# Kernel tuning notes

Measured on AMD Instinct MI355X. Metric: run time of the kernel, lower is better.

Reference implementation:

```python
import jax, jax.numpy as jnp
import numpy as np

N_NODES = 100000
N_EDGES = 1600000
EMB = 128
EDGE_DIMS = [6, 3]
BN_EPS = 1e-5


def setup_inputs() -> dict:
    key = jax.random.key(0)
    ks = jax.random.split(key, 16)
    inp = {
        "node_feats": jax.random.normal(ks[0], (N_NODES, EMB), jnp.float32),
        "edge_feat_0": jax.random.uniform(ks[1], (N_EDGES, EDGE_DIMS[0]), jnp.float32),
        "edge_feat_1": jax.random.uniform(ks[2], (N_EDGES, EDGE_DIMS[1]), jnp.float32),
        "src": jax.random.randint(ks[3], (N_EDGES,), 0, N_NODES, jnp.int32),
        "dst": jax.random.randint(ks[4], (N_EDGES,), 0, N_NODES, jnp.int32),
    }
    # edge embedding linears (MLP num_layers==1 -> plain Linear)
    s0 = 1.0 / np.sqrt(EDGE_DIMS[0])
    s1 = 1.0 / np.sqrt(EDGE_DIMS[1])
    inp["We0"] = jax.random.uniform(ks[5], (EDGE_DIMS[0], EMB), jnp.float32, -s0, s0)
    inp["be0"] = jax.random.uniform(ks[6], (EMB,), jnp.float32, -s0, s0)
    inp["We1"] = jax.random.uniform(ks[7], (EDGE_DIMS[1], EMB), jnp.float32, -s1, s1)
    inp["be1"] = jax.random.uniform(ks[8], (EMB,), jnp.float32, -s1, s1)
    # mlp: Linear(emb, 2*emb) -> ReLU -> Linear(2*emb, emb)
    sm = 1.0 / np.sqrt(EMB)
    sh = 1.0 / np.sqrt(2 * EMB)
    inp["W1"] = jax.random.uniform(ks[9], (EMB, 2 * EMB), jnp.float32, -sm, sm)
    inp["b1"] = jax.random.uniform(ks[10], (2 * EMB,), jnp.float32, -sm, sm)
    inp["W2"] = jax.random.uniform(ks[11], (2 * EMB, EMB), jnp.float32, -sh, sh)
    inp["b2"] = jax.random.uniform(ks[12], (EMB,), jnp.float32, -sh, sh)
    # batch norm affine params
    inp["gamma"] = jnp.ones((EMB,), jnp.float32)
    inp["beta"] = jnp.zeros((EMB,), jnp.float32)
    return inp


def reference(node_feats, edge_feat_0, edge_feat_1, src, dst,
              We0, be0, We1, be1, W1, b1, W2, b2, gamma, beta):
    n_nodes = node_feats.shape[0]
    # per-family edge embeddings, summed
    edge_embs = (edge_feat_0 @ We0 + be0) + (edge_feat_1 @ We1 + be1)  # [E, D]
    # u_add_e: gather src node feats, add edge emb
    msgs = node_feats[src] + edge_embs  # [E, D]
    # scatter-sum to destination nodes
    agg = jax.ops.segment_sum(msgs, dst, num_segments=n_nodes)  # [N, D]
    # MLP: Linear -> ReLU -> Linear
    h = jax.nn.relu(agg @ W1 + b1) @ W2 + b2  # [N, D]
    # BatchNorm1d (training mode: batch statistics, biased variance)
    mean = jnp.mean(h, axis=0)
    var = jnp.var(h, axis=0)
    h = (h - mean) * jax.lax.rsqrt(var + BN_EPS) * gamma + beta
    return h
```

## Files before the change

### kernel.cpp

```cpp
#include <hip/hip_runtime.h>

#define N_NODES 100000
#define N_EDGES 1600000
#define EMB 128
#define BM 16
#define NSLAB 64
#define BN_EPS 1e-5f

#define SCAN_BLK 512
#define NB_SCAN ((N_NODES + SCAN_BLK - 1) / SCAN_BLK)
#define NPAD (NB_SCAN * SCAN_BLK)

typedef short short8 __attribute__((ext_vector_type(8)));
typedef float floatx4 __attribute__((ext_vector_type(4)));

__device__ __forceinline__ ushort f2bf(float x) {
    unsigned u = __float_as_uint(x);
    u += 0x7fffu + ((u >> 16) & 1u);
    return (ushort)(u >> 16);
}
__device__ __forceinline__ float lo2f(unsigned p) {
    return __uint_as_float(p << 16);
}
__device__ __forceinline__ float hi2f(unsigned p) {
    return __uint_as_float(p & 0xffff0000u);
}

#define DPP_ADD(x, ctrl, mask) \
    ((x) + __int_as_float(__builtin_amdgcn_update_dpp(0, __float_as_int(x), ctrl, mask, 0xf, true)))

__device__ __forceinline__ float wave_sum63(float x) {
    x = DPP_ADD(x, 0x111, 0xf);
    x = DPP_ADD(x, 0x112, 0xf);
    x = DPP_ADD(x, 0x114, 0xf);
    x = DPP_ADD(x, 0x118, 0xf);
    x = DPP_ADD(x, 0x142, 0xa);
    x = DPP_ADD(x, 0x143, 0xc);
    return __int_as_float(__builtin_amdgcn_readlane(__float_as_int(x), 63));
}

__global__ __launch_bounds__(256) void setup_kernel(
    const float* __restrict__ nf, ushort* __restrict__ nfbf,
    const int* __restrict__ dst, int* __restrict__ counts,
    const float* __restrict__ W1, const float* __restrict__ W2,
    ushort* __restrict__ w1f, ushort* __restrict__ w2f)
{
    int gtid = blockIdx.x * 256 + threadIdx.x;
    long gstride = (long)gridDim.x * 256;

    if (gtid < 65536) {
        int idx = gtid;
        int i = idx & 7;
        int lane = (idx >> 3) & 63;
        int kloc = ((lane >> 4) << 3) + i;
        int nloc = lane & 15;
        if (idx < 32768) {
            int ks = (idx >> 9) & 3, nt = idx >> 11;
            w1f[idx] = f2bf(W1[(ks * 32 + kloc) * 256 + nt * 16 + nloc]);
        } else {
            int j = idx - 32768;
            int ks = (j >> 9) & 7, nt = j >> 12;
            w2f[j] = f2bf(W2[(ks * 32 + kloc) * 128 + nt * 16 + nloc]);
        }
    }

    long total = (long)N_NODES * EMB / 4;
    for (long p = gtid; p < total; p += gstride) {
        float4 v = ((const float4*)nf)[p];
        ushort4 o;
        o.x = f2bf(v.x); o.y = f2bf(v.y); o.z = f2bf(v.z); o.w = f2bf(v.w);
        ((ushort4*)nfbf)[p] = o;
    }

    for (long e = gtid; e < N_EDGES; e += gstride)
        atomicAdd(&counts[dst[e]], 1);
}

__global__ __launch_bounds__(SCAN_BLK) void scan_blocksum_kernel(
    const int* __restrict__ counts, int* __restrict__ blockSums)
{
    __shared__ int red[SCAN_BLK];
    int t = threadIdx.x;
    int i = blockIdx.x * SCAN_BLK + t;
    red[t] = (i < N_NODES) ? counts[i] : 0;
    __syncthreads();
    for (int s = SCAN_BLK / 2; s > 0; s >>= 1) {
        if (t < s) red[t] += red[t + s];
        __syncthreads();
    }
    if (t == 0) blockSums[blockIdx.x] = red[0];
}

__global__ __launch_bounds__(SCAN_BLK) void scan_final_kernel(
    const int* __restrict__ counts, const int* __restrict__ blockSums,
    int* __restrict__ offsets, int* __restrict__ cursor)
{
    __shared__ int s[SCAN_BLK];
    __shared__ int bs[256];
    int t = threadIdx.x;
    if (t < 256) bs[t] = (t < NB_SCAN) ? blockSums[t] : 0;
    __syncthreads();
    for (int off = 1; off < 256; off <<= 1) {
        int v = (t < 256 && t >= off) ? bs[t - off] : 0;
        __syncthreads();
        if (t < 256) bs[t] += v;
        __syncthreads();
    }
    int blockBase = (blockIdx.x == 0) ? 0 : bs[blockIdx.x - 1];

    int i = blockIdx.x * SCAN_BLK + t;
    int orig = (i < N_NODES) ? counts[i] : 0;
    s[t] = orig;
    __syncthreads();
    for (int off = 1; off < SCAN_BLK; off <<= 1) {
        int v = (t >= off) ? s[t - off] : 0;
        __syncthreads();
        s[t] += v;
        __syncthreads();
    }
    int excl = s[t] - orig + blockBase;
    if (i < N_NODES) { offsets[i] = excl; cursor[i] = excl; }
    if (i == N_NODES) offsets[N_NODES] = N_EDGES;
}

__global__ __launch_bounds__(256) void scatter24_kernel(
    const int* __restrict__ src, const int* __restrict__ dst,
    const float* __restrict__ ef0, const float* __restrict__ ef1,
    int* __restrict__ cursor, int* __restrict__ rec24)
{
    int e = blockIdx.x * 256 + threadIdx.x;
    if (e >= N_EDGES) return;
    int t = dst[e];
    int pos = atomicAdd(&cursor[t], 1);

    const float2* p0 = (const float2*)(ef0 + (long)e * 6);
    float2 q0 = p0[0], q1 = p0[1], q2 = p0[2];
    const float* p1 = ef1 + (long)e * 3;
    float g0 = p1[0], g1 = p1[1], g2 = p1[2];

    unsigned u0 = (unsigned)f2bf(q0.x) | ((unsigned)f2bf(q0.y) << 16);
    unsigned u1 = (unsigned)f2bf(q1.x) | ((unsigned)f2bf(q1.y) << 16);
    unsigned u2 = (unsigned)f2bf(q2.x) | ((unsigned)f2bf(q2.y) << 16);
    unsigned u3 = (unsigned)f2bf(g0)   | ((unsigned)f2bf(g1) << 16);
    unsigned u4 = (unsigned)f2bf(g2);

    int2* out = (int2*)(rec24 + (long)pos * 6);
    out[0] = make_int2(src[e], (int)u0);
    out[1] = make_int2((int)u1, (int)u2);
    out[2] = make_int2((int)u3, (int)u4);
}

__device__ __forceinline__ void gather_full_chunks(
    int& base, int end, int lane, int q, int lp,
    const int* __restrict__ rec24, const int4* __restrict__ nf16,
    float4& accA, float4& accB, float* fs)
{
    for (; base + 64 <= end; base += 64) {
        const int2* rp = (const int2*)(rec24 + (long)(base + lane) * 6);
        int2 ra = rp[0], rb = rp[1], rc = rp[2];
        int sid = ra.x;
        fs[0] += lo2f((unsigned)ra.y); fs[1] += hi2f((unsigned)ra.y);
        fs[2] += lo2f((unsigned)rb.x); fs[3] += hi2f((unsigned)rb.x);
        fs[4] += lo2f((unsigned)rb.y); fs[5] += hi2f((unsigned)rb.y);
        fs[6] += lo2f((unsigned)rc.x); fs[7] += hi2f((unsigned)rc.x);
        fs[8] += lo2f((unsigned)rc.y);
#pragma unroll 4
        for (int j = 0; j < 16; ++j) {
            int s = __shfl(sid, 4 * j + q);
            int4 nv = nf16[(long)s * 16 + lp];
            accA.x += lo2f((unsigned)nv.x); accA.y += hi2f((unsigned)nv.x);
            accA.z += lo2f((unsigned)nv.y); accA.w += hi2f((unsigned)nv.y);
            accB.x += lo2f((unsigned)nv.z); accB.y += hi2f((unsigned)nv.z);
            accB.z += lo2f((unsigned)nv.w); accB.w += hi2f((unsigned)nv.w);
        }
    }
}

__global__ __launch_bounds__(256, 8) void gather4_kernel(
    const ushort* __restrict__ nfbf, const int* __restrict__ rec24,
    const int* __restrict__ offsets,
    const float* __restrict__ We0, const float* __restrict__ be0,
    const float* __restrict__ We1, const float* __restrict__ be1,
    float* __restrict__ agg)
{
    int wv = threadIdx.x >> 6, lane = threadIdx.x & 63;
    int n0 = blockIdx.x * 8 + wv * 2;
    int q = lane >> 4, lp = lane & 15;
    const int4* nf16 = (const int4*)nfbf;

    int beg0 = offsets[n0];
    int mid  = offsets[n0 + 1];
    int end1 = offsets[n0 + 2];

    float4 a0A = make_float4(0.f, 0.f, 0.f, 0.f), a0B = a0A;
    float4 a1A = a0A, a1B = a0A;
    float fs0[9] = {}, fs1[9] = {};

    int b0 = beg0, b1 = mid;
    gather_full_chunks(b0, mid, lane, q, lp, rec24, nf16, a0A, a0B, fs0);
    gather_full_chunks(b1, end1, lane, q, lp, rec24, nf16, a1A, a1B, fs1);

    int m0 = mid - b0, m1 = end1 - b1;
    int sid0 = 0, sid1 = 0;
    if (lane < m0) {
        const int2* rp = (const int2*)(rec24 + (long)(b0 + lane) * 6);
        int2 ra = rp[0], rb = rp[1], rc = rp[2];
        sid0 = ra.x;
        fs0[0] += lo2f((unsigned)ra.y); fs0[1] += hi2f((unsigned)ra.y);
        fs0[2] += lo2f((unsigned)rb.x); fs0[3] += hi2f((unsigned)rb.x);
        fs0[4] += lo2f((unsigned)rb.y); fs0[5] += hi2f((unsigned)rb.y);
        fs0[6] += lo2f((unsigned)rc.x); fs0[7] += hi2f((unsigned)rc.x);
        fs0[8] += lo2f((unsigned)rc.y);
    }
    if (lane < m1) {
        const int2* rp = (const int2*)(rec24 + (long)(b1 + lane) * 6);
        int2 ra = rp[0], rb = rp[1], rc = rp[2];
        sid1 = ra.x;
        fs1[0] += lo2f((unsigned)ra.y); fs1[1] += hi2f((unsigned)ra.y);
        fs1[2] += lo2f((unsigned)rb.x); fs1[3] += hi2f((unsigned)rb.x);
        fs1[4] += lo2f((unsigned)rb.y); fs1[5] += hi2f((unsigned)rb.y);
        fs1[6] += lo2f((unsigned)rc.x); fs1[7] += hi2f((unsigned)rc.x);
        fs1[8] += lo2f((unsigned)rc.y);
    }
    int mx = m0 > m1 ? m0 : m1;
    int rounds = (mx + 3) >> 2;
#pragma unroll 4
    for (int j = 0; j < rounds; ++j) {
        int r = 4 * j + q;
        int s0 = __shfl(sid0, r);
        int s1 = __shfl(sid1, r);
        if (r < m0) {
            int4 nv = nf16[(long)s0 * 16 + lp];
            a0A.x += lo2f((unsigned)nv.x); a0A.y += hi2f((unsigned)nv.x);
            a0A.z += lo2f((unsigned)nv.y); a0A.w += hi2f((unsigned)nv.y);
            a0B.x += lo2f((unsigned)nv.z); a0B.y += hi2f((unsigned)nv.z);
            a0B.z += lo2f((unsigned)nv.w); a0B.w += hi2f((unsigned)nv.w);
        }
        if (r < m1) {
            int4 nv = nf16[(long)s1 * 16 + lp];
            a1A.x += lo2f((unsigned)nv.x); a1A.y += hi2f((unsigned)nv.x);
            a1A.z += lo2f((unsigned)nv.y); a1A.w += hi2f((unsigned)nv.y);
            a1B.x += lo2f((unsigned)nv.z); a1B.y += hi2f((unsigned)nv.z);
            a1B.z += lo2f((unsigned)nv.w); a1B.w += hi2f((unsigned)nv.w);
        }
    }

#define QRED(v) v += __shfl_xor(v, 16); v += __shfl_xor(v, 32);
    QRED(a0A.x) QRED(a0A.y) QRED(a0A.z) QRED(a0A.w)
    QRED(a0B.x) QRED(a0B.y) QRED(a0B.z) QRED(a0B.w)
    QRED(a1A.x) QRED(a1A.y) QRED(a1A.z) QRED(a1A.w)
    QRED(a1B.x) QRED(a1B.y) QRED(a1B.z) QRED(a1B.w)
#undef QRED

    float fk0[9], fk1[9];
#pragma unroll
    for (int k = 0; k < 9; ++k) {
        fk0[k] = wave_sum63(fs0[k]);
        fk1[k] = wave_sum63(fs1[k]);
    }

    int nodesel = q & 1;
    int hh = q >> 1;
    long myn = (long)n0 + nodesel;
    float deg = nodesel ? (float)(end1 - mid) : (float)(mid - beg0);
    float4 acc;
    {
        float4 selA, selB;
        selA.x = nodesel ? a1A.x : a0A.x; selA.y = nodesel ? a1A.y : a0A.y;
        selA.z = nodesel ? a1A.z : a0A.z; selA.w = nodesel ? a1A.w : a0A.w;
        selB.x = nodesel ? a1B.x : a0B.x; selB.y = nodesel ? a1B.y : a0B.y;
        selB.z = nodesel ? a1B.z : a0B.z; selB.w = nodesel ? a1B.w : a0B.w;
        acc.x = hh ? selB.x : selA.x; acc.y = hh ? selB.y : selA.y;
        acc.z = hh ? selB.z : selA.z; acc.w = hh ? selB.w : selA.w;
    }
    int fidx = 2 * lp + hh;
    float4 bb0 = ((const float4*)be0)[fidx];
    float4 bb1 = ((const float4*)be1)[fidx];
    float4 e;
    e.x = deg * (bb0.x + bb1.x); e.y = deg * (bb0.y + bb1.y);
    e.z = deg * (bb0.z + bb1.z); e.w = deg * (bb0.w + bb1.w);
#pragma unroll
    for (int k = 0; k < 6; ++k) {
        float f = nodesel ? fk1[k] : fk0[k];
        float4 w = ((const float4*)We0)[k * 32 + fidx];
        e.x = fmaf(f, w.x, e.x); e.y = fmaf(f, w.y, e.y);
        e.z = fmaf(f, w.z, e.z); e.w = fmaf(f, w.w, e.w);
    }
#pragma unroll
    for (int k = 0; k < 3; ++k) {
        float f = nodesel ? fk1[6 + k] : fk0[6 + k];
        float4 w = ((const float4*)We1)[k * 32 + fidx];
        e.x = fmaf(f, w.x, e.x); e.y = fmaf(f, w.y, e.y);
        e.z = fmaf(f, w.z, e.z); e.w = fmaf(f, w.w, e.w);
    }
    float4 o = make_float4(acc.x + e.x, acc.y + e.y, acc.z + e.z, acc.w + e.w);
    ((float4*)agg)[myn * 32 + fidx] = o;
}

__global__ __launch_bounds__(256) void edge_scatter_kernel(
    const float* __restrict__ node_feats,
    const float* __restrict__ ef0,
    const float* __restrict__ ef1,
    const int* __restrict__ src,
    const int* __restrict__ dst,
    const float* __restrict__ We0, const float* __restrict__ be0,
    const float* __restrict__ We1, const float* __restrict__ be1,
    float* __restrict__ agg)
{
    __shared__ float wS[10 * EMB];
    int tid = threadIdx.x;
    for (int i = tid; i < 6 * EMB; i += 256) wS[i] = We0[i];
    for (int i = tid; i < 3 * EMB; i += 256) wS[6 * EMB + i] = We1[i];
    if (tid < EMB) wS[9 * EMB + tid] = be0[tid] + be1[tid];
    __syncthreads();

    int e = blockIdx.x * 2 + (tid >> 7);
    if (e >= N_EDGES) return;
    int d = tid & 127;
    int s = src[e];
    int t = dst[e];
    const float* f0 = ef0 + (long)e * 6;
    const float* f1 = ef1 + (long)e * 3;

    float emb = wS[9 * EMB + d];
#pragma unroll
    for (int k = 0; k < 6; ++k) emb = fmaf(f0[k], wS[k * EMB + d], emb);
#pragma unroll
    for (int k = 0; k < 3; ++k) emb = fmaf(f1[k], wS[6 * EMB + k * EMB + d], emb);

    float val = node_feats[(long)s * EMB + d] + emb;
    atomicAdd(&agg[(long)t * EMB + d], val);
}

__global__ __launch_bounds__(256) void mlp_mfma_kernel(
    const float* __restrict__ aggf, ushort* __restrict__ hbf,
    const ushort* __restrict__ w1f, const ushort* __restrict__ w2f,
    const float* __restrict__ b1, const float* __restrict__ b2,
    float* __restrict__ stats)
{
    __shared__ __align__(16) char h1S[32 * 512];

    int tid = threadIdx.x;
    int lane = tid & 63;
    int wv = tid >> 6;
    long base = (long)blockIdx.x * 32;

    short8 a[2][4];
#pragma unroll
    for (int mt = 0; mt < 2; ++mt)
#pragma unroll
        for (int ks = 0; ks < 4; ++ks) {
            long row = base + mt * 16 + (lane & 15);
            const float4* p = (const float4*)(aggf + row * EMB + ks * 32 + ((lane >> 4) << 3));
            float4 x = p[0], y = p[1];
            union { ushort u[8]; short8 v; } pk;
            pk.u[0] = f2bf(x.x); pk.u[1] = f2bf(x.y); pk.u[2] = f2bf(x.z); pk.u[3] = f2bf(x.w);
            pk.u[4] = f2bf(y.x); pk.u[5] = f2bf(y.y); pk.u[6] = f2bf(y.z); pk.u[7] = f2bf(y.w);
            a[mt][ks] = pk.v;
        }

    floatx4 acc1[2][4];
#pragma unroll
    for (int nt = 0; nt < 4; ++nt) {
        float bias = b1[(wv * 4 + nt) * 16 + (lane & 15)];
#pragma unroll
        for (int mt = 0; mt < 2; ++mt)
            acc1[mt][nt] = (floatx4){bias, bias, bias, bias};
    }
#pragma unroll
    for (int ks = 0; ks < 4; ++ks) {
#pragma unroll
        for (int nt = 0; nt < 4; ++nt) {
            short8 b = *(const short8*)&w1f[(((wv * 4 + nt) * 4 + ks) * 64 + lane) * 8];
            acc1[0][nt] = __builtin_amdgcn_mfma_f32_16x16x32_bf16(a[0][ks], b, acc1[0][nt], 0, 0, 0);
            acc1[1][nt] = __builtin_amdgcn_mfma_f32_16x16x32_bf16(a[1][ks], b, acc1[1][nt], 0, 0, 0);
        }
    }
#pragma unroll
    for (int mt = 0; mt < 2; ++mt)
#pragma unroll
        for (int nt = 0; nt < 4; ++nt)
#pragma unroll
            for (int i = 0; i < 4; ++i) {
                int row = mt * 16 + ((lane >> 4) << 2) + i;
                int col = (wv * 4 + nt) * 16 + (lane & 15);
                float v = fmaxf(acc1[mt][nt][i], 0.f);
                *(ushort*)&h1S[row * 512 + ((2 * col) ^ ((row & 7) << 4))] = f2bf(v);
            }
    __syncthreads();

    int swz = (lane & 7) << 4;
    floatx4 acc2[2][2];
#pragma unroll
    for (int nt = 0; nt < 2; ++nt) {
        float bias = b2[(wv * 2 + nt) * 16 + (lane & 15)];
#pragma unroll
        for (int mt = 0; mt < 2; ++mt)
            acc2[mt][nt] = (floatx4){bias, bias, bias, bias};
    }
#pragma unroll
    for (int ks = 0; ks < 8; ++ks) {
        int kb = ks * 64 + ((lane >> 4) << 4);
        short8 a0 = *(const short8*)&h1S[(lane & 15) * 512 + (kb ^ swz)];
        short8 a1 = *(const short8*)&h1S[(16 + (lane & 15)) * 512 + (kb ^ swz)];
#pragma unroll
        for (int nt = 0; nt < 2; ++nt) {
            short8 b = *(const short8*)&w2f[(((wv * 2 + nt) * 8 + ks) * 64 + lane) * 8];
            acc2[0][nt] = __builtin_amdgcn_mfma_f32_16x16x32_bf16(a0, b, acc2[0][nt], 0, 0, 0);
            acc2[1][nt] = __builtin_amdgcn_mfma_f32_16x16x32_bf16(a1, b, acc2[1][nt], 0, 0, 0);
        }
    }

    float s[2] = {0.f, 0.f}, s2[2] = {0.f, 0.f};
#pragma unroll
    for (int nt = 0; nt < 2; ++nt) {
        int col = (wv * 2 + nt) * 16 + (lane & 15);
#pragma unroll
        for (int mt = 0; mt < 2; ++mt)
#pragma unroll
            for (int i = 0; i < 4; ++i) {
                int row = mt * 16 + ((lane >> 4) << 2) + i;
                float v = acc2[mt][nt][i];
                hbf[(base + row) * EMB + col] = f2bf(v);
                s[nt] += v;
                s2[nt] = fmaf(v, v, s2[nt]);
            }
    }
#pragma unroll
    for (int nt = 0; nt < 2; ++nt) {
        s[nt] += __shfl_xor(s[nt], 16);
        s[nt] += __shfl_xor(s[nt], 32);
        s2[nt] += __shfl_xor(s2[nt], 16);
        s2[nt] += __shfl_xor(s2[nt], 32);
    }
    if (lane < 16) {
        float* slab = stats + (blockIdx.x & (NSLAB - 1)) * (2 * EMB);
#pragma unroll
        for (int nt = 0; nt < 2; ++nt) {
            int col = (wv * 2 + nt) * 16 + lane;
            atomicAdd(&slab[col], s[nt]);
            atomicAdd(&slab[EMB + col], s2[nt]);
        }
    }
}

__global__ __launch_bounds__(256) void mlp_kernel(
    float* __restrict__ h,
    const float* __restrict__ W1, const float* __restrict__ b1,
    const float* __restrict__ W2, const float* __restrict__ b2,
    float* __restrict__ stats)
{
    __shared__ float aggS[BM][EMB];
    __shared__ float h1S[BM][2 * EMB];
    __shared__ float sredS[256];
    __shared__ float s2redS[256];

    int tid = threadIdx.x;
    long base = (long)blockIdx.x * BM;

    for (int i = tid; i < BM * EMB; i += 256)
        aggS[i >> 7][i & 127] = h[base * EMB + i];
    __syncthreads();

    {
        float acc[BM];
        float bias = b1[tid];
#pragma unroll
        for (int r = 0; r < BM; ++r) acc[r] = bias;
        for (int k = 0; k < EMB; ++k) {
            float w = W1[k * (2 * EMB) + tid];
#pragma unroll
            for (int r = 0; r < BM; ++r) acc[r] = fmaf(aggS[r][k], w, acc[r]);
        }
#pragma unroll
        for (int r = 0; r < BM; ++r) h1S[r][tid] = fmaxf(acc[r], 0.0f);
    }
    __syncthreads();

    {
        int c = tid & 127;
        int half = tid >> 7;
        float acc[8];
        float bias = b2[c];
#pragma unroll
        for (int r = 0; r < 8; ++r) acc[r] = bias;
        for (int k = 0; k < 2 * EMB; ++k) {
            float w = W2[k * EMB + c];
#pragma unroll
            for (int r = 0; r < 8; ++r) acc[r] = fmaf(h1S[half * 8 + r][k], w, acc[r]);
        }
        float s = 0.f, s2 = 0.f;
#pragma unroll
        for (int r = 0; r < 8; ++r) {
            h[(base + half * 8 + r) * EMB + c] = acc[r];
            s += acc[r];
            s2 = fmaf(acc[r], acc[r], s2);
        }
        sredS[tid] = s;
        s2redS[tid] = s2;
    }
    __syncthreads();
    if (tid < 128) {
        float s = sredS[tid] + sredS[tid + 128];
        float s2 = s2redS[tid] + s2redS[tid + 128];
        float* slab = stats + (blockIdx.x & (NSLAB - 1)) * (2 * EMB);
        atomicAdd(&slab[tid], s);
        atomicAdd(&slab[EMB + tid], s2);
    }
}

__global__ __launch_bounds__(256) void bn_apply_bf16_kernel(
    const ushort* __restrict__ hbf, float* __restrict__ out,
    const float* __restrict__ stats,
    const float* __restrict__ gamma, const float* __restrict__ beta)
{
    __shared__ float scS[EMB], shS[EMB];
    int tid = threadIdx.x;
    if (tid < EMB) {
        float s = 0.f, s2 = 0.f;
        for (int b = 0; b < NSLAB; ++b) {
            s += stats[b * (2 * EMB) + tid];
            s2 += stats[b * (2 * EMB) + EMB + tid];
        }
        float mean = s / (float)N_NODES;
        float var = s2 / (float)N_NODES - mean * mean;
        float sc = gamma[tid] * rsqrtf(var + BN_EPS);
        scS[tid] = sc;
        shS[tid] = beta[tid] - mean * sc;
    }
    __syncthreads();
    long total = (long)N_NODES * EMB / 8;
    long stride = (long)gridDim.x * blockDim.x;
    for (long p = (long)blockIdx.x * blockDim.x + threadIdx.x; p < total; p += stride) {
        uint4 v = ((const uint4*)hbf)[p];
        int c = (int)((p * 8) & 127);
        float4 o1, o2;
        o1.x = fmaf(lo2f(v.x), scS[c + 0], shS[c + 0]);
        o1.y = fmaf(hi2f(v.x), scS[c + 1], shS[c + 1]);
        o1.z = fmaf(lo2f(v.y), scS[c + 2], shS[c + 2]);
        o1.w = fmaf(hi2f(v.y), scS[c + 3], shS[c + 3]);
        o2.x = fmaf(lo2f(v.z), scS[c + 4], shS[c + 4]);
        o2.y = fmaf(hi2f(v.z), scS[c + 5], shS[c + 5]);
        o2.z = fmaf(lo2f(v.w), scS[c + 6], shS[c + 6]);
        o2.w = fmaf(hi2f(v.w), scS[c + 7], shS[c + 7]);
        ((float4*)out)[2 * p] = o1;
        ((float4*)out)[2 * p + 1] = o2;
    }
}

__global__ __launch_bounds__(256) void bn_apply_fused_kernel(
    float* __restrict__ h, const float* __restrict__ stats,
    const float* __restrict__ gamma, const float* __restrict__ beta)
{
    __shared__ float scS[EMB], shS[EMB];
    int tid = threadIdx.x;
    if (tid < EMB) {
        float s = 0.f, s2 = 0.f;
        for (int b = 0; b < NSLAB; ++b) {
            s += stats[b * (2 * EMB) + tid];
            s2 += stats[b * (2 * EMB) + EMB + tid];
        }
        float mean = s / (float)N_NODES;
        float var = s2 / (float)N_NODES - mean * mean;
        float sc = gamma[tid] * rsqrtf(var + BN_EPS);
        scS[tid] = sc;
        shS[tid] = beta[tid] - mean * sc;
    }
    __syncthreads();
    long total = (long)N_NODES * EMB / 4;
    long stride = (long)gridDim.x * blockDim.x;
    for (long i = (long)blockIdx.x * blockDim.x + threadIdx.x; i < total; i += stride) {
        float4 v = ((float4*)h)[i];
        int c = (int)((i * 4) & 127);
        v.x = fmaf(v.x, scS[c + 0], shS[c + 0]);
        v.y = fmaf(v.y, scS[c + 1], shS[c + 1]);
        v.z = fmaf(v.z, scS[c + 2], shS[c + 2]);
        v.w = fmaf(v.w, scS[c + 3], shS[c + 3]);
        ((float4*)h)[i] = v;
    }
}

extern "C" void kernel_launch(void* const* d_in, const int* in_sizes, int n_in,
                              void* d_out, int out_size, void* d_ws, size_t ws_size,
                              hipStream_t stream) {
    const float* node_feats = (const float*)d_in[0];
    const float* ef0 = (const float*)d_in[1];
    const float* ef1 = (const float*)d_in[2];
    const int* src = (const int*)d_in[3];
    const int* dst = (const int*)d_in[4];
    const float* We0 = (const float*)d_in[5];
    const float* be0 = (const float*)d_in[6];
    const float* We1 = (const float*)d_in[7];
    const float* be1 = (const float*)d_in[8];
    const float* W1 = (const float*)d_in[9];
    const float* b1 = (const float*)d_in[10];
    const float* W2 = (const float*)d_in[11];
    const float* b2 = (const float*)d_in[12];
    const float* gamma = (const float*)d_in[13];
    const float* beta = (const float*)d_in[14];

    float* out = (float*)d_out;

    float* stats = (float*)d_ws;
    float* scaleshift = stats + NSLAB * 2 * EMB;
    int* counts = (int*)(scaleshift + 256);
    int* offsets = counts + NPAD;
    int* cursor = offsets + NPAD;
    int* blockSums = cursor + NPAD;
    ushort* w1f = (ushort*)(blockSums + 256);
    ushort* w2f = w1f + 32768;
    int* rec24 = (int*)(w2f + 32768);
    ushort* hbf = (ushort*)rec24;
    ushort* nfbf = (ushort*)(rec24 + (size_t)N_EDGES * 6);
    size_t needed = (size_t)((char*)(nfbf + (size_t)N_NODES * EMB) - (char*)d_ws);

    if (ws_size >= needed) {
        hipMemsetAsync(d_ws, 0,
            (size_t)(NSLAB * 2 * EMB + 256) * sizeof(float) + (size_t)NPAD * sizeof(int),
            stream);
        setup_kernel<<<2048, 256, 0, stream>>>(
            node_feats, nfbf, dst, counts, W1, W2, w1f, w2f);
        scan_blocksum_kernel<<<NB_SCAN, SCAN_BLK, 0, stream>>>(counts, blockSums);
        scan_final_kernel<<<NB_SCAN, SCAN_BLK, 0, stream>>>(counts, blockSums, offsets, cursor);
        scatter24_kernel<<<(N_EDGES + 255) / 256, 256, 0, stream>>>(
            src, dst, ef0, ef1, cursor, rec24);
        gather4_kernel<<<N_NODES / 8, 256, 0, stream>>>(
            nfbf, rec24, offsets, We0, be0, We1, be1, out);
        mlp_mfma_kernel<<<N_NODES / 32, 256, 0, stream>>>(
            out, hbf, w1f, w2f, b1, b2, stats);
        bn_apply_bf16_kernel<<<1024, 256, 0, stream>>>(hbf, out, stats, gamma, beta);
    } else {
        hipMemsetAsync(stats, 0, (size_t)NSLAB * 2 * EMB * sizeof(float), stream);
        hipMemsetAsync(d_out, 0, (size_t)N_NODES * EMB * sizeof(float), stream);
        edge_scatter_kernel<<<N_EDGES / 2, 256, 0, stream>>>(
            node_feats, ef0, ef1, src, dst, We0, be0, We1, be1, out);
        mlp_kernel<<<N_NODES / BM, 256, 0, stream>>>(out, W1, b1, W2, b2, stats);
        bn_apply_fused_kernel<<<4096, 256, 0, stream>>>(out, stats, gamma, beta);
    }
}
```

Baseline: 317.4 us.

## Store aggregate as bf16 and pad edge records to 32 bytes for vector loads

The gather kernel now writes the aggregated node features as bf16 instead of fp32, and the MLP kernel loads them directly as packed bf16 operands without converting. This halves the intermediate's write and read traffic and drops the conversion work in the MLP. Separately, when the workspace is large enough, edge records are padded from 24 to 32 bytes so they can be written and read with one 16-byte plus one 8-byte access instead of three 8-byte accesses, at the cost of more record bytes moved. Rounding to bf16 happens at the same point as before, so precision is unchanged, though the bf16 aggregate reuses the output buffer.

```diff
diff --git a/kernel.cpp b/kernel.cpp
--- a/kernel.cpp
+++ b/kernel.cpp
@@ -123,10 +123,11 @@
     if (i == N_NODES) offsets[N_NODES] = N_EDGES;
 }
 
-__global__ __launch_bounds__(256) void scatter24_kernel(
+template<int RS>
+__global__ __launch_bounds__(256) void scatter_kernel_t(
     const int* __restrict__ src, const int* __restrict__ dst,
     const float* __restrict__ ef0, const float* __restrict__ ef1,
-    int* __restrict__ cursor, int* __restrict__ rec24)
+    int* __restrict__ cursor, int* __restrict__ rec)
 {
     int e = blockIdx.x * 256 + threadIdx.x;
     if (e >= N_EDGES) return;
@@ -138,32 +139,54 @@
     const float* p1 = ef1 + (long)e * 3;
     float g0 = p1[0], g1 = p1[1], g2 = p1[2];
 
-    unsigned u0 = (unsigned)f2bf(q0.x) | ((unsigned)f2bf(q0.y) << 16);
-    unsigned u1 = (unsigned)f2bf(q1.x) | ((unsigned)f2bf(q1.y) << 16);
-    unsigned u2 = (unsigned)f2bf(q2.x) | ((unsigned)f2bf(q2.y) << 16);
-    unsigned u3 = (unsigned)f2bf(g0)   | ((unsigned)f2bf(g1) << 16);
-    unsigned u4 = (unsigned)f2bf(g2);
-
-    int2* out = (int2*)(rec24 + (long)pos * 6);
-    out[0] = make_int2(src[e], (int)u0);
-    out[1] = make_int2((int)u1, (int)u2);
-    out[2] = make_int2((int)u3, (int)u4);
-}
-
+    int u0 = (int)((unsigned)f2bf(q0.x) | ((unsigned)f2bf(q0.y) << 16));
+    int u1 = (int)((unsigned)f2bf(q1.x) | ((unsigned)f2bf(q1.y) << 16));
+    int u2 = (int)((unsigned)f2bf(q2.x) | ((unsigned)f2bf(q2.y) << 16));
+    int u3 = (int)((unsigned)f2bf(g0)   | ((unsigned)f2bf(g1) << 16));
+    int u4 = (int)((unsigned)f2bf(g2));
+
+    int* out = rec + (long)pos * RS;
+    if constexpr (RS == 8) {
+        ((int4*)out)[0] = make_int4(src[e], u0, u1, u2);
+        ((int2*)out)[2] = make_int2(u3, u4);
+    } else {
+        ((int2*)out)[0] = make_int2(src[e], u0);
+        ((int2*)out)[1] = make_int2(u1, u2);
+        ((int2*)out)[2] = make_int2(u3, u4);
+    }
+}
+
+template<int RS>
+__device__ __forceinline__ int read_rec(const int* __restrict__ rec, long pos,
+                                        float* fs) {
+    const int* p = rec + pos * RS;
+    int sid; unsigned w1, w2, w3, w4, w5;
+    if constexpr (RS == 8) {
+        int4 a = *(const int4*)p;
+        int2 b = *(const int2*)(p + 4);
+        sid = a.x; w1 = (unsigned)a.y; w2 = (unsigned)a.z; w3 = (unsigned)a.w;
+        w4 = (unsigned)b.x; w5 = (unsigned)b.y;
+    } else {
+        int2 a = ((const int2*)p)[0], b = ((const int2*)p)[1], c = ((const int2*)p)[2];
+        sid = a.x; w1 = (unsigned)a.y; w2 = (unsigned)b.x; w3 = (unsigned)b.y;
+        w4 = (unsigned)c.x; w5 = (unsigned)c.y;
+    }
+    fs[0] += lo2f(w1); fs[1] += hi2f(w1);
+    fs[2] += lo2f(w2); fs[3] += hi2f(w2);
+    fs[4] += lo2f(w3); fs[5] += hi2f(w3);
+    fs[6] += lo2f(w4); fs[7] += hi2f(w4);
+    fs[8] += lo2f(w5);
+    return sid;
+}
+
+template<int RS>
 __device__ __forceinline__ void gather_full_chunks(
     int& base, int end, int lane, int q, int lp,
-    const int* __restrict__ rec24, const int4* __restrict__ nf16,
+    const int* __restrict__ rec, const int4* __restrict__ nf16,
     float4& accA, float4& accB, float* fs)
 {
     for (; base + 64 <= end; base += 64) {
-        const int2* rp = (const int2*)(rec24 + (long)(base + lane) * 6);
-        int2 ra = rp[0], rb = rp[1], rc = rp[2];
-        int sid = ra.x;
-        fs[0] += lo2f((unsigned)ra.y); fs[1] += hi2f((unsigned)ra.y);
-        fs[2] += lo2f((unsigned)rb.x); fs[3] += hi2f((unsigned)rb.x);
-        fs[4] += lo2f((unsigned)rb.y); fs[5] += hi2f((unsigned)rb.y);
-        fs[6] += lo2f((unsigned)rc.x); fs[7] += hi2f((unsigned)rc.x);
-        fs[8] += lo2f((unsigned)rc.y);
+        int sid = read_rec<RS>(rec, (long)(base + lane), fs);
 #pragma unroll 4
         for (int j = 0; j < 16; ++j) {
             int s = __shfl(sid, 4 * j + q);
@@ -176,12 +199,13 @@
     }
 }
 
-__global__ __launch_bounds__(256, 8) void gather4_kernel(
-    const ushort* __restrict__ nfbf, const int* __restrict__ rec24,
+template<int RS>
+__global__ __launch_bounds__(256, 8) void gather_kernel_t(
+    const ushort* __restrict__ nfbf, const int* __restrict__ rec,
     const int* __restrict__ offsets,
     const float* __restrict__ We0, const float* __restrict__ be0,
     const float* __restrict__ We1, const float* __restrict__ be1,
-    float* __restrict__ agg)
+    ushort* __restrict__ aggbf)
 {
     int wv = threadIdx.x >> 6, lane = threadIdx.x & 63;
     int n0 = blockIdx.x * 8 + wv * 2;
@@ -197,31 +221,14 @@
     float fs0[9] = {}, fs1[9] = {};
 
     int b0 = beg0, b1 = mid;
-    gather_full_chunks(b0, mid, lane, q, lp, rec24, nf16, a0A, a0B, fs0);
-    gather_full_chunks(b1, end1, lane, q, lp, rec24, nf16, a1A, a1B, fs1);
+    gather_full_chunks<RS>(b0, mid, lane, q, lp, rec, nf16, a0A, a0B, fs0);
+    gather_full_chunks<RS>(b1, end1, lane, q, lp, rec, nf16, a1A, a1B, fs1);
 
     int m0 = mid - b0, m1 = end1 - b1;
     int sid0 = 0, sid1 = 0;
-    if (lane < m0) {
-        const int2* rp = (const int2*)(rec24 + (long)(b0 + lane) * 6);
-        int2 ra = rp[0], rb = rp[1], rc = rp[2];
-        sid0 = ra.x;
-        fs0[0] += lo2f((unsigned)ra.y); fs0[1] += hi2f((unsigned)ra.y);
-        fs0[2] += lo2f((unsigned)rb.x); fs0[3] += hi2f((unsigned)rb.x);
-        fs0[4] += lo2f((unsigned)rb.y); fs0[5] += hi2f((unsigned)rb.y);
-        fs0[6] += lo2f((unsigned)rc.x); fs0[7] += hi2f((unsigned)rc.x);
-        fs0[8] += lo2f((unsigned)rc.y);
-    }
-    if (lane < m1) {
-        const int2* rp = (const int2*)(rec24 + (long)(b1 + lane) * 6);
-        int2 ra = rp[0], rb = rp[1], rc = rp[2];
-        sid1 = ra.x;
-        fs1[0] += lo2f((unsigned)ra.y); fs1[1] += hi2f((unsigned)ra.y);
-        fs1[2] += lo2f((unsigned)rb.x); fs1[3] += hi2f((unsigned)rb.x);
-        fs1[4] += lo2f((unsigned)rb.y); fs1[5] += hi2f((unsigned)rb.y);
-        fs1[6] += lo2f((unsigned)rc.x); fs1[7] += hi2f((unsigned)rc.x);
-        fs1[8] += lo2f((unsigned)rc.y);
-    }
+    if (lane < m0) sid0 = read_rec<RS>(rec, (long)(b0 + lane), fs0);
+    if (lane < m1) sid1 = read_rec<RS>(rec, (long)(b1 + lane), fs1);
+
     int mx = m0 > m1 ? m0 : m1;
     int rounds = (mx + 3) >> 2;
 #pragma unroll 4
@@ -293,8 +300,10 @@
         e.x = fmaf(f, w.x, e.x); e.y = fmaf(f, w.y, e.y);
         e.z = fmaf(f, w.z, e.z); e.w = fmaf(f, w.w, e.w);
     }
-    float4 o = make_float4(acc.x + e.x, acc.y + e.y, acc.z + e.z, acc.w + e.w);
-    ((float4*)agg)[myn * 32 + fidx] = o;
+    ushort4 o;
+    o.x = f2bf(acc.x + e.x); o.y = f2bf(acc.y + e.y);
+    o.z = f2bf(acc.z + e.z); o.w = f2bf(acc.w + e.w);
+    ((ushort4*)aggbf)[myn * 32 + fidx] = o;
 }
 
 __global__ __launch_bounds__(256) void edge_scatter_kernel(
@@ -333,7 +342,7 @@
 }
 
 __global__ __launch_bounds__(256) void mlp_mfma_kernel(
-    const float* __restrict__ aggf, ushort* __restrict__ hbf,
+    const ushort* __restrict__ aggbf, ushort* __restrict__ hbf,
     const ushort* __restrict__ w1f, const ushort* __restrict__ w2f,
     const float* __restrict__ b1, const float* __restrict__ b2,
     float* __restrict__ stats)
@@ -351,12 +360,7 @@
 #pragma unroll
         for (int ks = 0; ks < 4; ++ks) {
             long row = base + mt * 16 + (lane & 15);
-            const float4* p = (const float4*)(aggf + row * EMB + ks * 32 + ((lane >> 4) << 3));
-            float4 x = p[0], y = p[1];
-            union { ushort u[8]; short8 v; } pk;
-            pk.u[0] = f2bf(x.x); pk.u[1] = f2bf(x.y); pk.u[2] = f2bf(x.z); pk.u[3] = f2bf(x.w);
-            pk.u[4] = f2bf(y.x); pk.u[5] = f2bf(y.y); pk.u[6] = f2bf(y.z); pk.u[7] = f2bf(y.w);
-            a[mt][ks] = pk.v;
+            a[mt][ks] = *(const short8*)&aggbf[row * EMB + ks * 32 + ((lane >> 4) << 3)];
         }
 
     floatx4 acc1[2][4];
@@ -600,6 +604,7 @@
     const float* beta = (const float*)d_in[14];
 
     float* out = (float*)d_out;
+    ushort* aggbf = (ushort*)d_out;
 
     float* stats = (float*)d_ws;
     float* scaleshift = stats + NSLAB * 2 * EMB;
@@ -609,12 +614,18 @@
     int* blockSums = cursor + NPAD;
     ushort* w1f = (ushort*)(blockSums + 256);
     ushort* w2f = w1f + 32768;
-    int* rec24 = (int*)(w2f + 32768);
-    ushort* hbf = (ushort*)rec24;
-    ushort* nfbf = (ushort*)(rec24 + (size_t)N_EDGES * 6);
-    size_t needed = (size_t)((char*)(nfbf + (size_t)N_NODES * EMB) - (char*)d_ws);
-
-    if (ws_size >= needed) {
+    int* rec = (int*)(w2f + 32768);
+    ushort* hbf = (ushort*)rec;
+
+    ushort* nfbfA = (ushort*)(rec + (size_t)N_EDGES * 8);
+    size_t needA = (size_t)((char*)(nfbfA + (size_t)N_NODES * EMB) - (char*)d_ws);
+    ushort* nfbfB = (ushort*)(rec + (size_t)N_EDGES * 6);
+    size_t needB = (size_t)((char*)(nfbfB + (size_t)N_NODES * EMB) - (char*)d_ws);
+
+    if (ws_size >= needB) {
+        bool tierA = (ws_size >= needA);
+        ushort* nfbf = tierA ? nfbfA : nfbfB;
+
         hipMemsetAsync(d_ws, 0,
             (size_t)(NSLAB * 2 * EMB + 256) * sizeof(float) + (size_t)NPAD * sizeof(int),
             stream);
@@ -622,12 +633,19 @@
             node_feats, nfbf, dst, counts, W1, W2, w1f, w2f);
         scan_blocksum_kernel<<<NB_SCAN, SCAN_BLK, 0, stream>>>(counts, blockSums);
         scan_final_kernel<<<NB_SCAN, SCAN_BLK, 0, stream>>>(counts, blockSums, offsets, cursor);
-        scatter24_kernel<<<(N_EDGES + 255) / 256, 256, 0, stream>>>(
-            src, dst, ef0, ef1, cursor, rec24);
-        gather4_kernel<<<N_NODES / 8, 256, 0, stream>>>(
-            nfbf, rec24, offsets, We0, be0, We1, be1, out);
+        if (tierA) {
+            scatter_kernel_t<8><<<(N_EDGES + 255) / 256, 256, 0, stream>>>(
+                src, dst, ef0, ef1, cursor, rec);
+            gather_kernel_t<8><<<N_NODES / 8, 256, 0, stream>>>(
+                nfbf, rec, offsets, We0, be0, We1, be1, aggbf);
+        } else {
+            scatter_kernel_t<6><<<(N_EDGES + 255) / 256, 256, 0, stream>>>(
+                src, dst, ef0, ef1, cursor, rec);
+            gather_kernel_t<6><<<N_NODES / 8, 256, 0, stream>>>(
+                nfbf, rec, offsets, We0, be0, We1, be1, aggbf);
+        }
         mlp_mfma_kernel<<<N_NODES / 32, 256, 0, stream>>>(
-            out, hbf, w1f, w2f, b1, b2, stats);
+            aggbf, hbf, w1f, w2f, b1, b2, stats);
         bn_apply_bf16_kernel<<<1024, 256, 0, stream>>>(hbf, out, stats, gamma, beta);
     } else {
         hipMemsetAsync(stats, 0, (size_t)NSLAB * 2 * EMB * sizeof(float), stream);
```

After: 321.7 us. Within noise of the previous version (+1.4%).
